# Optimization experiments

Measured on AMD Instinct MI355X. Metric: run time of the kernel, lower is better.

Reference implementation:

```python
import jax, jax.numpy as jnp
import numpy as np

HEADS = 12
HEAD_DIM = 64          # dim_out // heads = 768 // 12
Q_STRIDE = 4
WINDOW_SIZE = 16       # post-pool tokens per window; pre-pool = Q_STRIDE*WINDOW_SIZE = 64
DIM = 768
DIM_OUT = 768


def setup_inputs() -> dict:
    key = jax.random.key(0)
    k1, k2, k3 = jax.random.split(key, 3)
    B, N = 32, 3136
    x = jax.random.normal(k1, (B, N, DIM), dtype=jnp.float32)
    Wqkv = jax.random.normal(k2, (DIM, 3 * DIM_OUT), dtype=jnp.float32) * 0.02
    bqkv = jnp.zeros((3 * DIM_OUT,), dtype=jnp.float32)
    Wproj = jax.random.normal(k3, (DIM_OUT, DIM_OUT), dtype=jnp.float32) * 0.02
    bproj = jnp.zeros((DIM_OUT,), dtype=jnp.float32)
    return {"x": x, "Wqkv": Wqkv, "bqkv": bqkv, "Wproj": Wproj, "bproj": bproj}


def reference(x, Wqkv, bqkv, Wproj, bproj):
    B, N, _ = x.shape
    num_windows = N // (Q_STRIDE * WINDOW_SIZE)  # 49
    scale = HEAD_DIM ** (-0.5)

    # QKV projection (torch Linear uses x @ W^T; here Wqkv is stored [dim, 3*dim_out])
    qkv = x @ Wqkv + bqkv                                  # [B, N, 3*dim_out]
    # Same reshape as torch: windows are the inner split of the token axis
    qkv = qkv.reshape(B, N // num_windows, num_windows, 3, HEADS, HEAD_DIM)
    qkv = jnp.transpose(qkv, (3, 0, 4, 2, 1, 5))           # [3, B, h, w, t, d]
    q, k, v = qkv[0], qkv[1], qkv[2]                       # t = Q_STRIDE*WINDOW_SIZE

    # Query max-pooling over stride groups
    q = q.reshape(B, HEADS, num_windows, Q_STRIDE, WINDOW_SIZE, HEAD_DIM).max(axis=3)
    # q: [B, h, w, WINDOW_SIZE, d]

    # Scaled dot-product attention within each window
    logits = jnp.einsum('bhwqd,bhwkd->bhwqk', q, k) * scale
    attn = jax.nn.softmax(logits, axis=-1)
    o = jnp.einsum('bhwqk,bhwkd->bhwqd', attn, v)          # [B, h, w, q, d]

    # transpose(1,3) then flatten tokens, channels = heads*head_dim
    o = jnp.transpose(o, (0, 3, 2, 1, 4)).reshape(B, -1, DIM_OUT)
    return o @ Wproj + bproj
```

## Files before the change

### kernel.cpp

```cpp
#include <hip/hip_runtime.h>
#include <hip/hip_bf16.h>


typedef __bf16 bf16x8 __attribute__((ext_vector_type(8)));
typedef float f32x4 __attribute__((ext_vector_type(4)));
typedef unsigned short u16x8 __attribute__((ext_vector_type(8)));

#define GLOBAL_AS __attribute__((address_space(1)))
#define LDS_AS __attribute__((address_space(3)))

__device__ __forceinline__ unsigned short f2bf(float f) {
    unsigned u = __builtin_bit_cast(unsigned, f);
    u += 0x7FFFu + ((u >> 16) & 1u);
    return (unsigned short)(u >> 16);
}
__device__ __forceinline__ float bf2f(unsigned short h) {
    return __builtin_bit_cast(float, (unsigned)h << 16);
}

__device__ __forceinline__ void load16_to_lds(const void* g, void* l) {
    __builtin_amdgcn_global_load_lds((const GLOBAL_AS unsigned int*)g,
                                     (LDS_AS unsigned int*)l, 16, 0, 0);
}

__global__ void cvt_f32_bf16(const float* __restrict__ in,
                             unsigned short* __restrict__ out, long n4) {
    long i = (long)blockIdx.x * blockDim.x + threadIdx.x;
    if (i >= n4) return;
    float4 f = ((const float4*)in)[i];
    uint2 u;
    u.x = (unsigned)f2bf(f.x) | ((unsigned)f2bf(f.y) << 16);
    u.y = (unsigned)f2bf(f.z) | ((unsigned)f2bf(f.w) << 16);
    ((uint2*)out)[i] = u;
}

__global__ void transpose_cvt(const float* __restrict__ W,
                              unsigned short* __restrict__ Wt, int K, int N) {
    __shared__ float tile[32][33];
    int bx = blockIdx.x * 32;
    int by = blockIdx.y * 32;
    int tx = threadIdx.x & 31, ty = threadIdx.x >> 5;
    #pragma unroll
    for (int i = 0; i < 32; i += 8)
        tile[ty + i][tx] = W[(size_t)(by + ty + i) * N + bx + tx];
    __syncthreads();
    #pragma unroll
    for (int i = 0; i < 32; i += 8)
        Wt[(size_t)(bx + ty + i) * K + by + tx] = f2bf(tile[tx][ty + i]);
}

template <bool OUT_BF16>
__global__ __launch_bounds__(512, 2)
void gemm_bt256(const unsigned short* __restrict__ A,
                const unsigned short* __restrict__ Bt,
                const float* __restrict__ bias,
                void* __restrict__ Cv, int M, int N, int K) {
    __shared__ alignas(16) unsigned short lsA[2][256 * 64];
    __shared__ alignas(16) unsigned short lsB[2][256 * 64];

    const int tid  = threadIdx.x;
    const int lane = tid & 63;
    const int wave = tid >> 6;
    const int wm = (wave >> 2) * 128;
    const int wn = (wave & 3) * 64;

    const int nwg = (int)(gridDim.x * gridDim.y);
    const int hid = (int)(blockIdx.y * gridDim.x + blockIdx.x);
    const int q8  = nwg >> 3, r8 = nwg & 7;
    const int xcd = hid & 7;
    const int lid = (xcd < r8 ? xcd * (q8 + 1) : r8 * (q8 + 1) + (xcd - r8) * q8)
                    + (hid >> 3);
    const int tileX = lid % (int)gridDim.x;
    const int tileY = lid / (int)gridDim.x;
    const long bm = (long)tileY * 256;
    const long bn = (long)tileX * 256;

    const int arow  = tid >> 3;
    const int acolb = (((tid & 7) ^ (arow & 7)) * 16);
    const char* gA = (const char*)A + ((bm + arow) * (long)K) * 2 + acolb;
    const char* gB = (const char*)Bt + ((bn + arow) * (long)K) * 2 + acolb;
    const long rowStep = (long)K * 2 * 64;
    const int ldsWaveBase = wave * 512;

    f32x4 acc[8][4] = {};

    const int NT = K >> 6;

    auto STAGE = [&](int buf, int t) {
        const char* a = gA + (long)t * 128;
        const char* b = gB + (long)t * 128;
        #pragma unroll
        for (int it = 0; it < 4; ++it) {
            load16_to_lds(a + it * rowStep, &lsA[buf][it * 4096 + ldsWaveBase]);
            load16_to_lds(b + it * rowStep, &lsB[buf][it * 4096 + ldsWaveBase]);
        }
    };

    STAGE(0, 0);
    int cur = 0;
    const int lane15 = lane & 15;
    const int quad   = lane >> 4;

    for (int t = 0; t < NT; ++t) {
        __syncthreads();
        if (t + 1 < NT) STAGE(cur ^ 1, t + 1);
        #pragma unroll
        for (int ks = 0; ks < 64; ks += 32) {
            bf16x8 af[8], bg[4];
            const int colSwz = (ks + quad * 8) ^ ((lane & 7) * 8);
            #pragma unroll
            for (int i = 0; i < 8; ++i)
                af[i] = *(const bf16x8*)&lsA[cur][(wm + i * 16 + lane15) * 64 + colSwz];
            #pragma unroll
            for (int j = 0; j < 4; ++j)
                bg[j] = *(const bf16x8*)&lsB[cur][(wn + j * 16 + lane15) * 64 + colSwz];
            #pragma unroll
            for (int i = 0; i < 8; ++i)
                #pragma unroll
                for (int j = 0; j < 4; ++j)
                    acc[i][j] = __builtin_amdgcn_mfma_f32_16x16x32_bf16(
                        bg[j], af[i], acc[i][j], 0, 0, 0);
        }
        cur ^= 1;
    }

    const long rbase = bm + wm + lane15;
    const int  cbase = (int)bn + wn + quad * 4;
    #pragma unroll
    for (int j = 0; j < 4; ++j) {
        const int col = cbase + j * 16;
        const float4 bv = *(const float4*)&bias[col];
        #pragma unroll
        for (int i = 0; i < 8; ++i) {
            const long row = rbase + i * 16;
            const size_t idx = (size_t)row * N + col;
            const float v0 = acc[i][j][0] + bv.x;
            const float v1 = acc[i][j][1] + bv.y;
            const float v2 = acc[i][j][2] + bv.z;
            const float v3 = acc[i][j][3] + bv.w;
            if constexpr (OUT_BF16) {
                ushort4 s;
                s.x = f2bf(v0); s.y = f2bf(v1); s.z = f2bf(v2); s.w = f2bf(v3);
                *(ushort4*)((unsigned short*)Cv + idx) = s;
            } else {
                float4 s;
                s.x = v0; s.y = v1; s.z = v2; s.w = v3;
                *(float4*)((float*)Cv + idx) = s;
            }
        }
    }
}

__global__ __launch_bounds__(256)
void attn_win_mfma(const unsigned short* __restrict__ qkv,
                   unsigned short* __restrict__ o) {
    const int hg = blockIdx.x;
    const int w  = blockIdx.y;
    const int b  = blockIdx.z;
    const int wave = threadIdx.x >> 6;
    const int lane = threadIdx.x & 63;
    const int h = hg * 4 + wave;
    const int l = lane & 15;
    const int quad = lane >> 4;

    __shared__ alignas(16) unsigned short vT[4][64 * 72];
    __shared__ alignas(16) unsigned short ps[4][16 * 72];

    const long tokStride = 49L * 2304;
    const long base = ((long)b * 3136 + w) * 2304 + h * 64;

    bf16x8 af[2];
    {
        const unsigned short* qr = qkv + base + (long)l * tokStride + quad * 8;
        float m0[8], m1[8];
        #pragma unroll
        for (int sg = 0; sg < 4; ++sg) {
            uint4 u0 = *(const uint4*)(qr + (long)sg * 16 * tokStride);
            uint4 u1 = *(const uint4*)(qr + (long)sg * 16 * tokStride + 32);
            const unsigned short* p0 = (const unsigned short*)&u0;
            const unsigned short* p1 = (const unsigned short*)&u1;
            #pragma unroll
            for (int e = 0; e < 8; ++e) {
                float f0 = bf2f(p0[e]), f1 = bf2f(p1[e]);
                if (sg == 0) { m0[e] = f0; m1[e] = f1; }
                else { m0[e] = fmaxf(m0[e], f0); m1[e] = fmaxf(m1[e], f1); }
            }
        }
        u16x8 a0, a1;
        #pragma unroll
        for (int e = 0; e < 8; ++e) {
            a0[e] = f2bf(m0[e] * 0.125f);
            a1[e] = f2bf(m1[e] * 0.125f);
        }
        af[0] = __builtin_bit_cast(bf16x8, a0);
        af[1] = __builtin_bit_cast(bf16x8, a1);
    }

    {
        const unsigned short* vr = qkv + base + (long)lane * tokStride + 1536;
        unsigned short* vw = &vT[wave][0];
        #pragma unroll
        for (int i = 0; i < 8; ++i) {
            uint4 u = *(const uint4*)(vr + i * 8);
            const unsigned short* pe = (const unsigned short*)&u;
            #pragma unroll
            for (int e = 0; e < 8; ++e)
                vw[(i * 8 + e) * 72 + lane] = pe[e];
        }
    }

    f32x4 Sc[4] = {};
    {
        bf16x8 bk0, bk1;
        #pragma unroll
        for (int tt = 0; tt < 4; ++tt) {
            const unsigned short* kr =
                qkv + base + (long)(tt * 16 + l) * tokStride + 768 + quad * 8;
            bk0 = __builtin_bit_cast(bf16x8, *(const uint4*)kr);
            bk1 = __builtin_bit_cast(bf16x8, *(const uint4*)(kr + 32));
            Sc[tt] = __builtin_amdgcn_mfma_f32_16x16x32_bf16(af[0], bk0, Sc[tt], 0, 0, 0);
            Sc[tt] = __builtin_amdgcn_mfma_f32_16x16x32_bf16(af[1], bk1, Sc[tt], 0, 0, 0);
        }
    }

    float pr[4][4];
    {
        #pragma unroll
        for (int r = 0; r < 4; ++r) {
            float mx = fmaxf(fmaxf(Sc[0][r], Sc[1][r]), fmaxf(Sc[2][r], Sc[3][r]));
            #pragma unroll
            for (int off = 1; off < 16; off <<= 1)
                mx = fmaxf(mx, __shfl_xor(mx, off));
            float sum = 0.f;
            #pragma unroll
            for (int tt = 0; tt < 4; ++tt) {
                pr[tt][r] = __expf(Sc[tt][r] - mx);
                sum += pr[tt][r];
            }
            #pragma unroll
            for (int off = 1; off < 16; off <<= 1)
                sum += __shfl_xor(sum, off);
            const float inv = 1.0f / sum;
            #pragma unroll
            for (int tt = 0; tt < 4; ++tt) pr[tt][r] *= inv;
        }
    }

    {
        unsigned short* pw = &ps[wave][0];
        #pragma unroll
        for (int r = 0; r < 4; ++r)
            #pragma unroll
            for (int tt = 0; tt < 4; ++tt)
                pw[(quad * 4 + r) * 72 + tt * 16 + l] = f2bf(pr[tt][r]);
    }

    f32x4 Oc[4] = {};
    {
        #pragma unroll
        for (int s = 0; s < 2; ++s) {
            bf16x8 ap = *(const bf16x8*)&ps[wave][l * 72 + s * 32 + quad * 8];
            #pragma unroll
            for (int tt = 0; tt < 4; ++tt) {
                bf16x8 bv = *(const bf16x8*)&vT[wave][(tt * 16 + l) * 72 + s * 32 + quad * 8];
                Oc[tt] = __builtin_amdgcn_mfma_f32_16x16x32_bf16(ap, bv, Oc[tt], 0, 0, 0);
            }
        }
    }

    {
        const long obase = ((long)b * 784 + (long)(quad * 4) * 49 + w) * 768 + h * 64 + l;
        #pragma unroll
        for (int tt = 0; tt < 4; ++tt)
            #pragma unroll
            for (int r = 0; r < 4; ++r)
                o[obase + (long)r * 49 * 768 + tt * 16] = f2bf(Oc[tt][r]);
    }
}

extern "C" void kernel_launch(void* const* d_in, const int* in_sizes, int n_in,
                              void* d_out, int out_size, void* d_ws, size_t ws_size,
                              hipStream_t stream) {
    const float* x     = (const float*)d_in[0];
    const float* Wqkv  = (const float*)d_in[1];
    const float* bqkv  = (const float*)d_in[2];
    const float* Wproj = (const float*)d_in[3];
    const float* bproj = (const float*)d_in[4];
    float* out = (float*)d_out;

    const long needed1 = (32L * 3136 * 768 + 32L * 3136 * 2304 +
                          25088L * 768 + 2304L * 768 + 768L * 768) * 2;
    const int C  = (ws_size >= (size_t)needed1) ? 1 : 4;
    const int CB = 32 / C;
    const long XC = (long)CB * 3136 * 768;
    const long QC = (long)CB * 3136 * 2304;

    char* p = (char*)d_ws;
    unsigned short* xb    = (unsigned short*)p; p += XC * 2;
    unsigned short* qkvb  = (unsigned short*)p; p += QC * 2;
    unsigned short* ob    = (unsigned short*)p; p += 25088L * 768 * 2;
    unsigned short* WqkvT = (unsigned short*)p; p += 2304L * 768 * 2;
    unsigned short* WprojT= (unsigned short*)p; p += 768L * 768 * 2;

    transpose_cvt<<<dim3(72, 24), 256, 0, stream>>>(Wqkv, WqkvT, 768, 2304);
    transpose_cvt<<<dim3(24, 24), 256, 0, stream>>>(Wproj, WprojT, 768, 768);

    const int M = CB * 3136;
    for (int c = 0; c < C; ++c) {
        cvt_f32_bf16<<<(int)(XC / 4 / 256), 256, 0, stream>>>(x + (size_t)c * XC, xb, XC / 4);
        gemm_bt256<true><<<dim3(9, M / 256), 512, 0, stream>>>(
            xb, WqkvT, bqkv, qkvb, M, 2304, 768);
        attn_win_mfma<<<dim3(3, 49, CB), 256, 0, stream>>>(
            qkvb, ob + (size_t)c * CB * 784 * 768);
    }
    gemm_bt256<false><<<dim3(3, 98), 512, 0, stream>>>(
        ob, WprojT, bproj, out, 25088, 768, 768);
}
```

Measured before the change: 1.178 ms.

## Restructure GEMM main loop into fine-grained phased pipeline with split LDS staging

Rewrites the bf16 GEMM inner loop into eight phases per two K-tiles. Each phase loads half of the A fragments, issues one slice of global-to-LDS prefetch, and waits on explicit vmcnt counters and barriers rather than a single syncthreads per tile. The LDS layout changes to 32-column half-K slabs with a new swizzle, and MFMA runs use setprio so waves keep issuing matrix ops while loads are in flight. The goal is finer overlap of memory loads with MFMA and fewer registers held for fragments. The cost is more barriers per tile and fragile manual waitcnt logic, and NT is assumed even.

```diff
diff --git a/kernel.cpp b/kernel.cpp
--- a/kernel.cpp
+++ b/kernel.cpp
@@ -49,20 +49,58 @@
         Wt[(size_t)(bx + ty + i) * K + by + tx] = f2bf(tile[tx][ty + i]);
 }
 
+#define VM_WAIT4 asm volatile("s_waitcnt vmcnt(4)" ::: "memory")
+#define VM_WAIT0 asm volatile("s_waitcnt vmcnt(0)" ::: "memory")
+
+#define GPHASE(BUF, KSR, IH, LOADBG, STG, WAITS) do {                        \
+    if (LOADBG) {                                                            \
+        const unsigned short* bb =                                           \
+            &ls[(BUF) * 32768 + 16384 + (KSR) * 8192 + colOff];              \
+        bg[0] = *(const bf16x8*)&bb[(wn +  0 + lane15) * 32];                \
+        bg[1] = *(const bf16x8*)&bb[(wn + 16 + lane15) * 32];                \
+        bg[2] = *(const bf16x8*)&bb[(wn + 32 + lane15) * 32];                \
+        bg[3] = *(const bf16x8*)&bb[(wn + 48 + lane15) * 32];                \
+    }                                                                        \
+    {                                                                        \
+        const unsigned short* ab =                                           \
+            &ls[(BUF) * 32768 + (KSR) * 8192 + colOff];                      \
+        af[0] = *(const bf16x8*)&ab[(wm + (IH)*64 +  0 + lane15) * 32];      \
+        af[1] = *(const bf16x8*)&ab[(wm + (IH)*64 + 16 + lane15) * 32];      \
+        af[2] = *(const bf16x8*)&ab[(wm + (IH)*64 + 32 + lane15) * 32];      \
+        af[3] = *(const bf16x8*)&ab[(wm + (IH)*64 + 48 + lane15) * 32];      \
+    }                                                                        \
+    STG;                                                                     \
+    WAITS;                                                                   \
+    __builtin_amdgcn_s_barrier();                                            \
+    asm volatile("s_waitcnt lgkmcnt(0)" ::: "memory");                       \
+    __builtin_amdgcn_sched_barrier(0);                                       \
+    __builtin_amdgcn_s_setprio(1);                                           \
+    _Pragma("unroll")                                                        \
+    for (int ii = 0; ii < 4; ++ii)                                           \
+        _Pragma("unroll")                                                    \
+        for (int j = 0; j < 4; ++j)                                          \
+            acc[(IH)*4 + ii][j] = __builtin_amdgcn_mfma_f32_16x16x32_bf16(   \
+                bg[j], af[ii], acc[(IH)*4 + ii][j], 0, 0, 0);                \
+    __builtin_amdgcn_s_setprio(0);                                           \
+    __builtin_amdgcn_s_barrier();                                            \
+} while (0)
+
 template <bool OUT_BF16>
 __global__ __launch_bounds__(512, 2)
 void gemm_bt256(const unsigned short* __restrict__ A,
                 const unsigned short* __restrict__ Bt,
                 const float* __restrict__ bias,
                 void* __restrict__ Cv, int M, int N, int K) {
-    __shared__ alignas(16) unsigned short lsA[2][256 * 64];
-    __shared__ alignas(16) unsigned short lsB[2][256 * 64];
+    __shared__ alignas(16) unsigned short ls[65536];
 
     const int tid  = threadIdx.x;
     const int lane = tid & 63;
     const int wave = tid >> 6;
     const int wm = (wave >> 2) * 128;
     const int wn = (wave & 3) * 64;
+    const int lane15 = lane & 15;
+    const int quad   = lane >> 4;
+    const int colOff = ((quad ^ (lane15 & 3)) * 8);
 
     const int nwg = (int)(gridDim.x * gridDim.y);
     const int hid = (int)(blockIdx.y * gridDim.x + blockIdx.x);
@@ -75,53 +113,50 @@
     const long bm = (long)tileY * 256;
     const long bn = (long)tileX * 256;
 
-    const int arow  = tid >> 3;
-    const int acolb = (((tid & 7) ^ (arow & 7)) * 16);
-    const char* gA = (const char*)A + ((bm + arow) * (long)K) * 2 + acolb;
-    const char* gB = (const char*)Bt + ((bn + arow) * (long)K) * 2 + acolb;
-    const long rowStep = (long)K * 2 * 64;
+    const int r0 = tid >> 2;
+    const int lc = (tid & 3) ^ (r0 & 3);
+    const unsigned short* gA0 = A  + (bm + r0)       * (long)K + lc * 8;
+    const unsigned short* gA1 = A  + (bm + r0 + 128) * (long)K + lc * 8;
+    const unsigned short* gB0 = Bt + (bn + r0)       * (long)K + lc * 8;
+    const unsigned short* gB1 = Bt + (bn + r0 + 128) * (long)K + lc * 8;
     const int ldsWaveBase = wave * 512;
 
+    auto STAGE = [&](int buf, int op, int ksr, int kt) {
+        const int ko = kt * 64 + ksr * 32;
+        unsigned short* d = &ls[buf * 32768 + op * 16384 + ksr * 8192 + ldsWaveBase];
+        if (op == 0) {
+            load16_to_lds(gA0 + ko, d);
+            load16_to_lds(gA1 + ko, d + 4096);
+        } else {
+            load16_to_lds(gB0 + ko, d);
+            load16_to_lds(gB1 + ko, d + 4096);
+        }
+    };
+
     f32x4 acc[8][4] = {};
+    bf16x8 af[4], bg[4];
 
     const int NT = K >> 6;
-
-    auto STAGE = [&](int buf, int t) {
-        const char* a = gA + (long)t * 128;
-        const char* b = gB + (long)t * 128;
-        #pragma unroll
-        for (int it = 0; it < 4; ++it) {
-            load16_to_lds(a + it * rowStep, &lsA[buf][it * 4096 + ldsWaveBase]);
-            load16_to_lds(b + it * rowStep, &lsB[buf][it * 4096 + ldsWaveBase]);
-        }
-    };
-
-    STAGE(0, 0);
-    int cur = 0;
-    const int lane15 = lane & 15;
-    const int quad   = lane >> 4;
-
-    for (int t = 0; t < NT; ++t) {
-        __syncthreads();
-        if (t + 1 < NT) STAGE(cur ^ 1, t + 1);
-        #pragma unroll
-        for (int ks = 0; ks < 64; ks += 32) {
-            bf16x8 af[8], bg[4];
-            const int colSwz = (ks + quad * 8) ^ ((lane & 7) * 8);
-            #pragma unroll
-            for (int i = 0; i < 8; ++i)
-                af[i] = *(const bf16x8*)&lsA[cur][(wm + i * 16 + lane15) * 64 + colSwz];
-            #pragma unroll
-            for (int j = 0; j < 4; ++j)
-                bg[j] = *(const bf16x8*)&lsB[cur][(wn + j * 16 + lane15) * 64 + colSwz];
-            #pragma unroll
-            for (int i = 0; i < 8; ++i)
-                #pragma unroll
-                for (int j = 0; j < 4; ++j)
-                    acc[i][j] = __builtin_amdgcn_mfma_f32_16x16x32_bf16(
-                        bg[j], af[i], acc[i][j], 0, 0, 0);
-        }
-        cur ^= 1;
+    const int NI = NT >> 1;
+
+    STAGE(0, 0, 0, 0); STAGE(0, 1, 0, 0); STAGE(0, 0, 1, 0); STAGE(0, 1, 1, 0);
+    STAGE(1, 0, 0, 1); STAGE(1, 1, 0, 1);
+    VM_WAIT4;
+    __builtin_amdgcn_s_barrier();
+
+    for (int i = 0; i < NI; ++i) {
+        const int t2 = 2 * i;
+        const bool last = (i == NI - 1);
+        GPHASE(0, 0, 0, 1, { STAGE(1, 0, 1, t2 + 1); }, { (void)0; });
+        GPHASE(0, 0, 1, 0, { STAGE(1, 1, 1, t2 + 1); }, { (void)0; });
+        GPHASE(0, 1, 0, 1, { if (!last) STAGE(0, 0, 0, t2 + 2); }, { (void)0; });
+        GPHASE(0, 1, 1, 0, { if (!last) STAGE(0, 1, 0, t2 + 2); },
+               { if (last) { VM_WAIT0; } else { VM_WAIT4; } });
+        GPHASE(1, 0, 0, 1, { if (!last) STAGE(0, 0, 1, t2 + 2); }, { (void)0; });
+        GPHASE(1, 0, 1, 0, { if (!last) STAGE(0, 1, 1, t2 + 2); }, { (void)0; });
+        GPHASE(1, 1, 0, 1, { if (!last) STAGE(1, 0, 0, t2 + 3); }, { (void)0; });
+        GPHASE(1, 1, 1, 0, { if (!last) { STAGE(1, 1, 0, t2 + 3); VM_WAIT4; } },
+               { (void)0; });
     }
 
     const long rbase = bm + wm + lane15;
```

Measured after the change: 1.104 ms. 1.07x faster.
